# Optimization experiments

Hardware: AMD Instinct MI355X
Metric: run time of the kernel (lower is better)

## Reference

```python
import jax, jax.numpy as jnp
import numpy as np

N_HEAD = 16
N_FEAT = 1024
D_K = N_FEAT // N_HEAD
B, S = 2, 2048


def setup_inputs() -> dict:
    key = jax.random.key(0)
    ks = jax.random.split(key, 13)
    s = 1.0 / np.sqrt(N_FEAT)
    return {
        "query": jax.random.normal(ks[0], (B, S, N_FEAT), jnp.float32),
        "key": jax.random.normal(ks[1], (B, S, N_FEAT), jnp.float32),
        "value": jax.random.normal(ks[2], (B, S, N_FEAT), jnp.float32),
        "mask": jax.random.randint(ks[3], (B, 1, S), 0, 2).astype(bool),
        "w_q": jax.random.uniform(ks[4], (N_FEAT, N_FEAT), jnp.float32, -s, s),
        "b_q": jax.random.uniform(ks[5], (N_FEAT,), jnp.float32, -s, s),
        "w_k": jax.random.uniform(ks[6], (N_FEAT, N_FEAT), jnp.float32, -s, s),
        "b_k": jax.random.uniform(ks[7], (N_FEAT,), jnp.float32, -s, s),
        "w_v": jax.random.uniform(ks[8], (N_FEAT, N_FEAT), jnp.float32, -s, s),
        "b_v": jax.random.uniform(ks[9], (N_FEAT,), jnp.float32, -s, s),
        "w_o": jax.random.uniform(ks[10], (N_FEAT, N_FEAT), jnp.float32, -s, s),
        "b_o": jax.random.uniform(ks[11], (N_FEAT,), jnp.float32, -s, s),
    }


def reference(query, key, value, mask, w_q, b_q, w_k, b_k, w_v, b_v, w_o, b_o):
    b = query.shape[0]
    # projections -> [b, h, s, d_k]
    def proj(x, w, bias):
        y = x @ w.T + bias
        return y.reshape(b, -1, N_HEAD, D_K).transpose(0, 2, 1, 3)

    q = proj(query, w_q, b_q)
    k = proj(key, w_k, b_k)
    v = proj(value, w_v, b_v)

    scores = jnp.einsum("bhqd,bhkd->bhqk", q, k) / jnp.sqrt(jnp.asarray(D_K, q.dtype))
    m = mask[:, None]  # [b,1,1,s] broadcast over heads and query positions
    scores = jnp.where(m, jnp.asarray(-10000.0, scores.dtype), scores)
    attn = jax.nn.softmax(scores, axis=-1)
    attn = jnp.where(m, jnp.asarray(0.0, attn.dtype), attn)
    x = jnp.einsum("bhqk,bhkd->bhqd", attn, v)
    x = x.transpose(0, 2, 1, 3).reshape(b, -1, N_HEAD * D_K)
    return x @ w_o.T + b_o
```

## Files before the change

kernel.cpp:

```cpp
#include <hip/hip_runtime.h>
#include <hip/hip_bf16.h>


typedef float f32x4 __attribute__((ext_vector_type(4)));
typedef short bf16x8 __attribute__((ext_vector_type(8)));

typedef const __attribute__((address_space(1))) void* gas_ptr;
typedef __attribute__((address_space(3))) void* las_ptr;

#if __has_builtin(__builtin_amdgcn_exp2f)
#define EXP2(x) __builtin_amdgcn_exp2f(x)
#else
#define EXP2(x) exp2f(x)
#endif
#define LOG2E 1.4426950408889634f

static __device__ __forceinline__ short to_bf16s(float f) {
    __hip_bfloat16 h = __float2bfloat16(f);
    return __builtin_bit_cast(short, h);
}
static __device__ __forceinline__ unsigned cvtpk(float lo, float hi) {
    unsigned r;
    asm("v_cvt_pk_bf16_f32 %0, %1, %2" : "=v"(r) : "v"(lo), "v"(hi));
    return r;
}

__global__ void cvt3_kernel(const float* __restrict__ s0, const float* __restrict__ s1,
                            const float* __restrict__ s2, short* __restrict__ d0,
                            short* __restrict__ d1, short* __restrict__ d2) {
    const int g = blockIdx.x;
    const int sel = g >> 12;
    const int i = (g & 4095) * 256 + threadIdx.x;
    const float* s = sel == 0 ? s0 : (sel == 1 ? s1 : s2);
    short* d = sel == 0 ? d0 : (sel == 1 ? d1 : d2);
    float4 v = reinterpret_cast<const float4*>(s)[i];
    short4 o;
    o.x = to_bf16s(v.x); o.y = to_bf16s(v.y); o.z = to_bf16s(v.z); o.w = to_bf16s(v.w);
    reinterpret_cast<short4*>(d)[i] = o;
}
__global__ void cvt4_kernel(const float* __restrict__ s0, const float* __restrict__ s1,
                            const float* __restrict__ s2, const float* __restrict__ s3,
                            short* __restrict__ d0, short* __restrict__ d1,
                            short* __restrict__ d2, short* __restrict__ d3) {
    const int g = blockIdx.x;
    const int sel = g >> 10;
    const int i = (g & 1023) * 256 + threadIdx.x;
    const float* s = sel == 0 ? s0 : (sel == 1 ? s1 : (sel == 2 ? s2 : s3));
    short* d = sel == 0 ? d0 : (sel == 1 ? d1 : (sel == 2 ? d2 : d3));
    float4 v = reinterpret_cast<const float4*>(s)[i];
    short4 o;
    o.x = to_bf16s(v.x); o.y = to_bf16s(v.y); o.z = to_bf16s(v.z); o.w = to_bf16s(v.w);
    reinterpret_cast<short4*>(d)[i] = o;
}

__global__ void maskf_kernel(const int* __restrict__ mask, float* __restrict__ mf) {
    const int i = blockIdx.x * 256 + threadIdx.x;
    const int p = i & 31;
    const int phi = 8 * ((p >> 2) & 3) + 4 * (p >> 4) + (p & 3);
    mf[i] = mask[(i & ~31) | phi] ? (-10000.0f * LOG2E) : 0.0f;
}

static __device__ __forceinline__ void stage_tile(
    short* sa, short* sb, const short* A, const short* W,
    int m0, int n0, int k0, int tid)
{
#pragma unroll
    for (int rnd = 0; rnd < 2; ++rnd) {
        const int t = rnd * 256 + tid;
        const int c2 = t & 7;
        const int row = 2 * (t >> 3) + (c2 & 1);
        const int col = (c2 >> 1) * 8;
        __builtin_amdgcn_global_load_lds((gas_ptr)(A + (long)(m0 + row) * 1024 + k0 + col),
                                         (las_ptr)(sa + t * 8), 16, 0, 0);
        __builtin_amdgcn_global_load_lds((gas_ptr)(W + (long)(n0 + row) * 1024 + k0 + col),
                                         (las_ptr)(sb + t * 8), 16, 0, 0);
    }
}

static __device__ __forceinline__ void gemm_compute(
    const short* sa, const short* sb, int wr, int wc, int aoff, f32x4 (&acc)[4][4])
{
    bf16x8 af[4], bfr[4];
#pragma unroll
    for (int i = 0; i < 4; ++i)
        af[i] = *reinterpret_cast<const bf16x8*>(sa + (wr + i * 16) * 32 + aoff);
#pragma unroll
    for (int j = 0; j < 4; ++j)
        bfr[j] = *reinterpret_cast<const bf16x8*>(sb + (wc + j * 16) * 32 + aoff);
#pragma unroll
    for (int i = 0; i < 4; ++i)
#pragma unroll
        for (int j = 0; j < 4; ++j)
            acc[i][j] = __builtin_amdgcn_mfma_f32_16x16x32_bf16(af[i], bfr[j], acc[i][j], 0, 0, 0);
}

__global__ __launch_bounds__(256, 3) void proj_gemm(
    const short* __restrict__ A0, const short* __restrict__ A1, const short* __restrict__ A2,
    const short* __restrict__ W0, const short* __restrict__ W1, const short* __restrict__ W2,
    const float* __restrict__ bi0, const float* __restrict__ bi1, const float* __restrict__ bi2,
    short* __restrict__ o0, short* __restrict__ o1, short* __restrict__ o2)
{
    __shared__ __align__(16) short sa[2][4096];
    __shared__ __align__(16) short sb[2][4096];
    const int z = blockIdx.z;
    const short* A = z == 0 ? A0 : (z == 1 ? A1 : A2);
    const short* W = z == 0 ? W0 : (z == 1 ? W1 : W2);
    const float* bias = z == 0 ? bi0 : (z == 1 ? bi1 : bi2);
    short* outp = z == 0 ? o0 : (z == 1 ? o1 : o2);

    const int tid = threadIdx.x;
    const int w = tid >> 6, l = tid & 63;
    const int lr = l & 15, lh = l >> 4;
    const int m0 = blockIdx.x * 128, n0 = blockIdx.y * 128;
    const int wr = (w >> 1) * 64, wc = (w & 1) * 64;
    const int aoff = (lr >> 1) * 64 + (lr & 1) * 8 + lh * 16;

    f32x4 acc[4][4] = {};

    stage_tile(sa[0], sb[0], A, W, m0, n0, 0, tid);
    __syncthreads();
    for (int k0 = 0; k0 < 1024; k0 += 64) {
        stage_tile(sa[1], sb[1], A, W, m0, n0, k0 + 32, tid);
        gemm_compute(sa[0], sb[0], wr, wc, aoff, acc);
        __syncthreads();
        if (k0 + 64 < 1024)
            stage_tile(sa[0], sb[0], A, W, m0, n0, k0 + 64, tid);
        gemm_compute(sa[1], sb[1], wr, wc, aoff, acc);
        __syncthreads();
    }

    const float scl = (z == 0) ? 0.125f * LOG2E : 1.0f;
#pragma unroll
    for (int i = 0; i < 4; ++i) {
#pragma unroll
        for (int j = 0; j < 4; ++j) {
#pragma unroll
            for (int r = 0; r < 4; ++r) {
                const int row = m0 + wr + i * 16 + lh * 4 + r;
                const int col = n0 + wc + j * 16 + lr;
                const float v = (acc[i][j][r] + bias[col]) * scl;
                const int b = row >> 11, s = row & 2047;
                const int h = col >> 6, d = col & 63;
                if (z != 2)
                    outp[(((long)(b * 16 + h)) * 2048 + s) * 64 + d] = to_bf16s(v);
                else
                    outp[(((long)(b * 16 + h)) * 64 + d) * 2048 + s] = to_bf16s(v);
            }
        }
    }
}

__global__ __launch_bounds__(256, 2) void out_gemm(
    const short* __restrict__ A, const short* __restrict__ W,
    const float* __restrict__ bias, float* __restrict__ outp)
{
    __shared__ __align__(16) short sa[2][4096];
    __shared__ __align__(16) short sb[2][2048];
    const int tid = threadIdx.x;
    const int w = tid >> 6, l = tid & 63;
    const int lr = l & 15, lh = l >> 4;
    const int m0 = blockIdx.x * 128, n0 = blockIdx.y * 64;
    const int wr = (w >> 1) * 64, wc = (w & 1) * 32;
    const int aoff = (lr >> 1) * 64 + (lr & 1) * 8 + lh * 16;

    f32x4 acc[4][2] = {};

    const int c2 = tid & 7;
    const int brow = 2 * (tid >> 3) + (c2 & 1);
    const int bcol = (c2 >> 1) * 8;

    auto stage = [&](short* pa, short* pb, int k0) {
#pragma unroll
        for (int rnd = 0; rnd < 2; ++rnd) {
            const int t = rnd * 256 + tid;
            const int cc = t & 7;
            const int row = 2 * (t >> 3) + (cc & 1);
            const int col = (cc >> 1) * 8;
            __builtin_amdgcn_global_load_lds((gas_ptr)(A + (long)(m0 + row) * 1024 + k0 + col),
                                             (las_ptr)(pa + t * 8), 16, 0, 0);
        }
        __builtin_amdgcn_global_load_lds((gas_ptr)(W + (long)(n0 + brow) * 1024 + k0 + bcol),
                                         (las_ptr)(pb + tid * 8), 16, 0, 0);
    };
    auto compute = [&](const short* pa, const short* pb) {
        bf16x8 af[4], bfr[2];
#pragma unroll
        for (int i = 0; i < 4; ++i)
            af[i] = *reinterpret_cast<const bf16x8*>(pa + (wr + i * 16) * 32 + aoff);
#pragma unroll
        for (int j = 0; j < 2; ++j)
            bfr[j] = *reinterpret_cast<const bf16x8*>(pb + (wc + j * 16) * 32 + aoff);
#pragma unroll
        for (int i = 0; i < 4; ++i)
#pragma unroll
            for (int j = 0; j < 2; ++j)
                acc[i][j] = __builtin_amdgcn_mfma_f32_16x16x32_bf16(af[i], bfr[j], acc[i][j], 0, 0, 0);
    };

    stage(sa[0], sb[0], 0);
    __syncthreads();
    for (int k0 = 0; k0 < 1024; k0 += 64) {
        stage(sa[1], sb[1], k0 + 32);
        compute(sa[0], sb[0]);
        __syncthreads();
        if (k0 + 64 < 1024)
            stage(sa[0], sb[0], k0 + 64);
        compute(sa[1], sb[1]);
        __syncthreads();
    }

#pragma unroll
    for (int i = 0; i < 4; ++i)
#pragma unroll
        for (int j = 0; j < 2; ++j)
#pragma unroll
            for (int r = 0; r < 4; ++r) {
                const int row = m0 + wr + i * 16 + lh * 4 + r;
                const int col = n0 + wc + j * 16 + lr;
                outp[(long)row * 1024 + col] = acc[i][j][r] + bias[col];
            }
}


static __device__ __forceinline__ void stage_kv(
    short* ldsKb, short* ldsVb, const short* Kg, const short* Vg,
    int key0, int w, int srow, int prow, int schunk)
{
    __builtin_amdgcn_global_load_lds((gas_ptr)(Kg + (long)(key0 + prow) * 64 + schunk * 8),
                                     (las_ptr)(ldsKb + w * 512), 16, 0, 0);
    __builtin_amdgcn_global_load_lds((gas_ptr)(Kg + (long)(key0 + 32 + prow) * 64 + schunk * 8),
                                     (las_ptr)(ldsKb + 2048 + w * 512), 16, 0, 0);
    __builtin_amdgcn_global_load_lds((gas_ptr)(Vg + (long)srow * 2048 + key0 + schunk * 8),
                                     (las_ptr)(ldsVb + w * 512), 16, 0, 0);
    __builtin_amdgcn_global_load_lds((gas_ptr)(Vg + (long)(srow + 32) * 2048 + key0 + schunk * 8),
                                     (las_ptr)(ldsVb + 2048 + w * 512), 16, 0, 0);
}

static __device__ __forceinline__ void attn_step(
    const short* __restrict__ Kbuf, const short* __restrict__ Vbuf,
    const float* __restrict__ ldsM, int key0,
    const bf16x8 qf0, const bf16x8 qf1, int lr, int lh, int sw,
    float& mreg, float& lsum, f32x4 (&ao)[4])
{
    f32x4 mb[4];
#pragma unroll
    for (int s = 0; s < 4; ++s)
        mb[s] = *reinterpret_cast<const f32x4*>(ldsM + key0 + s * 16 + lh * 4);

    f32x4 sc[4];
#pragma unroll
    for (int s = 0; s < 4; ++s) {
        const short* kb = Kbuf + (s * 16 + lr) * 64;
        bf16x8 k0 = *reinterpret_cast<const bf16x8*>(kb + (((lh * 16) ^ sw) >> 1));
        bf16x8 k1 = *reinterpret_cast<const bf16x8*>(kb + (((64 + lh * 16) ^ sw) >> 1));
        sc[s] = __builtin_amdgcn_mfma_f32_16x16x32_bf16(k0, qf0, mb[s], 0, 0, 0);
        sc[s] = __builtin_amdgcn_mfma_f32_16x16x32_bf16(k1, qf1, sc[s], 0, 0, 0);
    }

    float m0 = fmaxf(fmaxf(fmaxf(sc[0][0], sc[0][1]), sc[0][2]), sc[0][3]);
    float m1 = fmaxf(fmaxf(fmaxf(sc[1][0], sc[1][1]), sc[1][2]), sc[1][3]);
    float m2 = fmaxf(fmaxf(fmaxf(sc[2][0], sc[2][1]), sc[2][2]), sc[2][3]);
    float m3 = fmaxf(fmaxf(fmaxf(sc[3][0], sc[3][1]), sc[3][2]), sc[3][3]);
    float t = fmaxf(fmaxf(m0, m1), fmaxf(m2, m3));
    t = fmaxf(t, __shfl_xor(t, 16));
    t = fmaxf(t, __shfl_xor(t, 32));
    if (__any(t > mreg + 8.0f)) {
        const float mn = fmaxf(mreg, t);
        const float sf = EXP2(mreg - mn);
        lsum *= sf;
#pragma unroll
        for (int d4 = 0; d4 < 4; ++d4) ao[d4] *= sf;
        mreg = mn;
    }
    float p[16], ps = 0.f;
#pragma unroll
    for (int s = 0; s < 4; ++s) {
#pragma unroll
        for (int r = 0; r < 4; ++r) {
            const float e = EXP2(sc[s][r] - mreg);
            p[s * 4 + r] = e;
            ps += e;
        }
    }
    ps += __shfl_xor(ps, 16);
    ps += __shfl_xor(ps, 32);
    lsum += ps;

    unsigned pw[8];
#pragma unroll
    for (int i = 0; i < 8; ++i) pw[i] = cvtpk(p[2 * i], p[2 * i + 1]);
    const bf16x8 pb0 = __builtin_bit_cast(bf16x8, *(ulonglong2*)&pw[0]);
    const bf16x8 pb1 = __builtin_bit_cast(bf16x8, *(ulonglong2*)&pw[4]);

#pragma unroll
    for (int c = 0; c < 2; ++c) {
        const bf16x8 pbc = c == 0 ? pb0 : pb1;
#pragma unroll
        for (int d4 = 0; d4 < 4; ++d4) {
            const short* vb = Vbuf + (d4 * 16 + lr) * 64;
            bf16x8 vf = *reinterpret_cast<const bf16x8*>(vb + (((c * 64 + lh * 16) ^ sw) >> 1));
            ao[d4] = __builtin_amdgcn_mfma_f32_16x16x32_bf16(vf, pbc, ao[d4], 0, 0, 0);
        }
    }
}

__global__ __launch_bounds__(256, 4) void attn_kernel(
    const short* __restrict__ Q, const short* __restrict__ Kmat,
    const short* __restrict__ Vt, const float* __restrict__ maskf,
    short* __restrict__ X)
{
    __shared__ __align__(16) short ldsK[2][4096];
    __shared__ __align__(16) short ldsV[2][4096];
    __shared__ __align__(16) float ldsM[2048];

    const int id = blockIdx.x;
    const int slot = id >> 3;
    const int bh = (id & 7) * 4 + (slot >> 5);
    const int q0 = (slot & 31) * 64;
    const int b = bh >> 4, h = bh & 15;
    const int w = threadIdx.x >> 6, l = threadIdx.x & 63;
    const int lr = l & 15, lh = l >> 4;
    const int sw = (lr & 7) << 4;

    const int srow = w * 8 + (l >> 3);
    const int schunk = (l & 7) ^ (srow & 7);
    const int prow = 8 * ((srow >> 2) & 3) + 4 * (srow >> 4) + (srow & 3);

    const short* Kg = Kmat + (long)bh * 2048 * 64;
    const short* Vg = Vt + (long)bh * 64 * 2048;

#pragma unroll
    for (int rnd = 0; rnd < 2; ++rnd) {
        const int t = rnd * 256 + threadIdx.x;
        __builtin_amdgcn_global_load_lds((gas_ptr)(maskf + (long)b * 2048 + t * 4),
                                         (las_ptr)(ldsM + t * 4), 16, 0, 0);
    }

    const short* Qp = Q + ((long)bh * 2048 + q0 + w * 16 + lr) * 64 + lh * 8;
    const bf16x8 qf0 = *reinterpret_cast<const bf16x8*>(Qp);
    const bf16x8 qf1 = *reinterpret_cast<const bf16x8*>(Qp + 32);

    float mreg = -1e30f, lsum = 0.f;
    f32x4 ao[4] = {};

    stage_kv(ldsK[0], ldsV[0], Kg, Vg, 0, w, srow, prow, schunk);
    __syncthreads();

    for (int tt = 0; tt < 16; ++tt) {
        const int key0 = tt * 128;
        stage_kv(ldsK[1], ldsV[1], Kg, Vg, key0 + 64, w, srow, prow, schunk);
        attn_step(ldsK[0], ldsV[0], ldsM, key0, qf0, qf1, lr, lh, sw, mreg, lsum, ao);
        __syncthreads();
        if (tt < 15)
            stage_kv(ldsK[0], ldsV[0], Kg, Vg, key0 + 128, w, srow, prow, schunk);
        attn_step(ldsK[1], ldsV[1], ldsM, key0 + 64, qf0, qf1, lr, lh, sw, mreg, lsum, ao);
        __syncthreads();
    }

    const float inv = 1.0f / fmaxf(lsum, 1e-30f);
    const int s = q0 + w * 16 + lr;
    short* Xp = X + ((long)b * 2048 + s) * 1024 + h * 64 + lh * 4;
#pragma unroll
    for (int d4 = 0; d4 < 4; ++d4) {
        uint2 o;
        o.x = cvtpk(ao[d4][0] * inv, ao[d4][1] * inv);
        o.y = cvtpk(ao[d4][2] * inv, ao[d4][3] * inv);
        *reinterpret_cast<uint2*>(Xp + d4 * 16) = o;
    }
}

extern "C" void kernel_launch(void* const* d_in, const int* in_sizes, int n_in,
                              void* d_out, int out_size, void* d_ws, size_t ws_size,
                              hipStream_t stream) {
    const float* query = (const float*)d_in[0];
    const float* key_  = (const float*)d_in[1];
    const float* value = (const float*)d_in[2];
    const int*   mask  = (const int*)d_in[3];
    const float* w_q = (const float*)d_in[4];
    const float* b_q = (const float*)d_in[5];
    const float* w_k = (const float*)d_in[6];
    const float* b_k = (const float*)d_in[7];
    const float* w_v = (const float*)d_in[8];
    const float* b_v = (const float*)d_in[9];
    const float* w_o = (const float*)d_in[10];
    const float* b_o = (const float*)d_in[11];

    const long SEQ = 4194304;
    const long WSZ = 1048576;
    short* ws = (short*)d_ws;
    short* cq = ws;
    short* ck = cq + SEQ;
    short* cv = ck + SEQ;
    short* wq = cv + SEQ;
    short* wk = wq + WSZ;
    short* wv = wk + WSZ;
    short* wo = wv + WSZ;
    short* Qb = wo + WSZ;
    short* Kb = Qb + SEQ;
    short* Vt = Kb + SEQ;
    short* Xb = cq;
    float* mkf = (float*)cv;

    cvt3_kernel<<<12288, 256, 0, stream>>>(query, key_, value, cq, ck, cv);
    cvt4_kernel<<<4096, 256, 0, stream>>>(w_q, w_k, w_v, w_o, wq, wk, wv, wo);

    dim3 blk(256);
    proj_gemm<<<dim3(32, 8, 3), blk, 0, stream>>>(cq, ck, cv, wq, wk, wv,
                                                  b_q, b_k, b_v, Qb, Kb, Vt);

    maskf_kernel<<<16, 256, 0, stream>>>(mask, mkf);

    attn_kernel<<<1024, blk, 0, stream>>>(Qb, Kb, Vt, mkf, Xb);

    out_gemm<<<dim3(32, 16), blk, 0, stream>>>(Xb, wo, b_o, (float*)d_out);
}
```

Measured before the change: 142.3 us.

## Transpose V projection output through LDS and prefetch mask into registers

The V projection epilogue previously wrote scattered 2-byte transposed stores. It now stages the tile transposed in shared memory and writes contiguous 4-byte rows along the sequence dimension for coalescing. The attention kernel drops its LDS mask buffer and loads mask values straight from global memory into registers, double-buffered alongside the K/V staging, which frees LDS and may raise occupancy. The softmax sums are also restructured into tree reductions to shorten dependency chains. The changes add an extra barrier and an enlarged shared array in proj_gemm, plus more registers in attn_kernel.

```diff
diff --git a/kernel.cpp b/kernel.cpp
--- a/kernel.cpp
+++ b/kernel.cpp
@@ -100,8 +100,12 @@
     const float* __restrict__ bi0, const float* __restrict__ bi1, const float* __restrict__ bi2,
     short* __restrict__ o0, short* __restrict__ o1, short* __restrict__ o2)
 {
-    __shared__ __align__(16) short sa[2][4096];
-    __shared__ __align__(16) short sb[2][4096];
+    __shared__ __align__(16) short smem[17408];
+    short* sA0 = smem;
+    short* sA1 = smem + 4096;
+    short* sB0 = smem + 8192;
+    short* sB1 = smem + 12288;
+
     const int z = blockIdx.z;
     const short* A = z == 0 ? A0 : (z == 1 ? A1 : A2);
     const short* W = z == 0 ? W0 : (z == 1 ? W1 : W2);
@@ -117,35 +121,59 @@
 
     f32x4 acc[4][4] = {};
 
-    stage_tile(sa[0], sb[0], A, W, m0, n0, 0, tid);
+    stage_tile(sA0, sB0, A, W, m0, n0, 0, tid);
     __syncthreads();
     for (int k0 = 0; k0 < 1024; k0 += 64) {
-        stage_tile(sa[1], sb[1], A, W, m0, n0, k0 + 32, tid);
-        gemm_compute(sa[0], sb[0], wr, wc, aoff, acc);
+        stage_tile(sA1, sB1, A, W, m0, n0, k0 + 32, tid);
+        gemm_compute(sA0, sB0, wr, wc, aoff, acc);
         __syncthreads();
         if (k0 + 64 < 1024)
-            stage_tile(sa[0], sb[0], A, W, m0, n0, k0 + 64, tid);
-        gemm_compute(sa[1], sb[1], wr, wc, aoff, acc);
-        __syncthreads();
-    }
-
-    const float scl = (z == 0) ? 0.125f * LOG2E : 1.0f;
-#pragma unroll
-    for (int i = 0; i < 4; ++i) {
-#pragma unroll
-        for (int j = 0; j < 4; ++j) {
-#pragma unroll
-            for (int r = 0; r < 4; ++r) {
-                const int row = m0 + wr + i * 16 + lh * 4 + r;
-                const int col = n0 + wc + j * 16 + lr;
-                const float v = (acc[i][j][r] + bias[col]) * scl;
-                const int b = row >> 11, s = row & 2047;
-                const int h = col >> 6, d = col & 63;
-                if (z != 2)
+            stage_tile(sA0, sB0, A, W, m0, n0, k0 + 64, tid);
+        gemm_compute(sA1, sB1, wr, wc, aoff, acc);
+        __syncthreads();
+    }
+
+    if (z != 2) {
+        const float scl = (z == 0) ? 0.125f * LOG2E : 1.0f;
+#pragma unroll
+        for (int i = 0; i < 4; ++i) {
+#pragma unroll
+            for (int j = 0; j < 4; ++j) {
+#pragma unroll
+                for (int r = 0; r < 4; ++r) {
+                    const int row = m0 + wr + i * 16 + lh * 4 + r;
+                    const int col = n0 + wc + j * 16 + lr;
+                    const float v = (acc[i][j][r] + bias[col]) * scl;
+                    const int b = row >> 11, s = row & 2047;
+                    const int h = col >> 6, d = col & 63;
                     outp[(((long)(b * 16 + h)) * 2048 + s) * 64 + d] = to_bf16s(v);
-                else
-                    outp[(((long)(b * 16 + h)) * 64 + d) * 2048 + s] = to_bf16s(v);
+                }
             }
+        }
+    } else {
+#pragma unroll
+        for (int i = 0; i < 4; ++i) {
+#pragma unroll
+            for (int j = 0; j < 4; ++j) {
+                const int dl = wc + j * 16 + lr;
+                const int sl = wr + i * 16 + lh * 4;
+                const float bv = bias[n0 + dl];
+                const unsigned w0 = cvtpk(acc[i][j][0] + bv, acc[i][j][1] + bv);
+                const unsigned w1 = cvtpk(acc[i][j][2] + bv, acc[i][j][3] + bv);
+                uint2 pr; pr.x = w0; pr.y = w1;
+                *reinterpret_cast<uint2*>(smem + dl * 136 + sl) = pr;
+            }
+        }
+        __syncthreads();
+        const int bb = m0 >> 11;
+        const int s0 = m0 & 2047;
+#pragma unroll 4
+        for (int rr = 0; rr < 32; ++rr) {
+            const int dl = w * 32 + rr;
+            const int col = n0 + dl;
+            const int hh = col >> 6, dd = col & 63;
+            const unsigned val = *reinterpret_cast<const unsigned*>(smem + dl * 136 + 2 * l);
+            *reinterpret_cast<unsigned*>(outp + ((long)(bb * 16 + hh) * 64 + dd) * 2048 + s0 + 2 * l) = val;
         }
     }
 }
@@ -238,15 +266,10 @@
 
 static __device__ __forceinline__ void attn_step(
     const short* __restrict__ Kbuf, const short* __restrict__ Vbuf,
-    const float* __restrict__ ldsM, int key0,
+    const f32x4 (&mb)[4],
     const bf16x8 qf0, const bf16x8 qf1, int lr, int lh, int sw,
     float& mreg, float& lsum, f32x4 (&ao)[4])
 {
-    f32x4 mb[4];
-#pragma unroll
-    for (int s = 0; s < 4; ++s)
-        mb[s] = *reinterpret_cast<const f32x4*>(ldsM + key0 + s * 16 + lh * 4);
-
     f32x4 sc[4];
 #pragma unroll
     for (int s = 0; s < 4; ++s) {
@@ -257,10 +280,10 @@
         sc[s] = __builtin_amdgcn_mfma_f32_16x16x32_bf16(k1, qf1, sc[s], 0, 0, 0);
     }
 
-    float m0 = fmaxf(fmaxf(fmaxf(sc[0][0], sc[0][1]), sc[0][2]), sc[0][3]);
-    float m1 = fmaxf(fmaxf(fmaxf(sc[1][0], sc[1][1]), sc[1][2]), sc[1][3]);
-    float m2 = fmaxf(fmaxf(fmaxf(sc[2][0], sc[2][1]), sc[2][2]), sc[2][3]);
-    float m3 = fmaxf(fmaxf(fmaxf(sc[3][0], sc[3][1]), sc[3][2]), sc[3][3]);
+    float m0 = fmaxf(fmaxf(sc[0][0], sc[0][1]), fmaxf(sc[0][2], sc[0][3]));
+    float m1 = fmaxf(fmaxf(sc[1][0], sc[1][1]), fmaxf(sc[1][2], sc[1][3]));
+    float m2 = fmaxf(fmaxf(sc[2][0], sc[2][1]), fmaxf(sc[2][2], sc[2][3]));
+    float m3 = fmaxf(fmaxf(sc[3][0], sc[3][1]), fmaxf(sc[3][2], sc[3][3]));
     float t = fmaxf(fmaxf(m0, m1), fmaxf(m2, m3));
     t = fmaxf(t, __shfl_xor(t, 16));
     t = fmaxf(t, __shfl_xor(t, 32));
@@ -272,23 +295,24 @@
         for (int d4 = 0; d4 < 4; ++d4) ao[d4] *= sf;
         mreg = mn;
     }
-    float p[16], ps = 0.f;
-#pragma unroll
-    for (int s = 0; s < 4; ++s) {
-#pragma unroll
-        for (int r = 0; r < 4; ++r) {
-            const float e = EXP2(sc[s][r] - mreg);
-            p[s * 4 + r] = e;
-            ps += e;
-        }
-    }
+    float e[16];
+#pragma unroll
+    for (int s = 0; s < 4; ++s)
+#pragma unroll
+        for (int r = 0; r < 4; ++r)
+            e[s * 4 + r] = EXP2(sc[s][r] - mreg);
+    const float e0 = (e[0] + e[1]) + (e[2] + e[3]);
+    const float e1 = (e[4] + e[5]) + (e[6] + e[7]);
+    const float e2 = (e[8] + e[9]) + (e[10] + e[11]);
+    const float e3 = (e[12] + e[13]) + (e[14] + e[15]);
+    float ps = (e0 + e1) + (e2 + e3);
     ps += __shfl_xor(ps, 16);
     ps += __shfl_xor(ps, 32);
     lsum += ps;
 
     unsigned pw[8];
 #pragma unroll
-    for (int i = 0; i < 8; ++i) pw[i] = cvtpk(p[2 * i], p[2 * i + 1]);
+    for (int i = 0; i < 8; ++i) pw[i] = cvtpk(e[2 * i], e[2 * i + 1]);
     const bf16x8 pb0 = __builtin_bit_cast(bf16x8, *(ulonglong2*)&pw[0]);
     const bf16x8 pb1 = __builtin_bit_cast(bf16x8, *(ulonglong2*)&pw[4]);
 
@@ -311,7 +335,6 @@
 {
     __shared__ __align__(16) short ldsK[2][4096];
     __shared__ __align__(16) short ldsV[2][4096];
-    __shared__ __align__(16) float ldsM[2048];
 
     const int id = blockIdx.x;
     const int slot = id >> 3;
@@ -328,13 +351,7 @@
 
     const short* Kg = Kmat + (long)bh * 2048 * 64;
     const short* Vg = Vt + (long)bh * 64 * 2048;
-
-#pragma unroll
-    for (int rnd = 0; rnd < 2; ++rnd) {
-        const int t = rnd * 256 + threadIdx.x;
-        __builtin_amdgcn_global_load_lds((gas_ptr)(maskf + (long)b * 2048 + t * 4),
-                                         (las_ptr)(ldsM + t * 4), 16, 0, 0);
-    }
+    const float* mfp = maskf + b * 2048 + lh * 4;
 
     const short* Qp = Q + ((long)bh * 2048 + q0 + w * 16 + lr) * 64 + lh * 8;
     const bf16x8 qf0 = *reinterpret_cast<const bf16x8*>(Qp);
@@ -343,17 +360,29 @@
     float mreg = -1e30f, lsum = 0.f;
     f32x4 ao[4] = {};
 
+    f32x4 mbA[4], mbB[4];
+#pragma unroll
+    for (int s = 0; s < 4; ++s)
+        mbA[s] = *reinterpret_cast<const f32x4*>(mfp + s * 16);
+
     stage_kv(ldsK[0], ldsV[0], Kg, Vg, 0, w, srow, prow, schunk);
     __syncthreads();
 
     for (int tt = 0; tt < 16; ++tt) {
         const int key0 = tt * 128;
+#pragma unroll
+        for (int s = 0; s < 4; ++s)
+            mbB[s] = *reinterpret_cast<const f32x4*>(mfp + key0 + 64 + s * 16);
         stage_kv(ldsK[1], ldsV[1], Kg, Vg, key0 + 64, w, srow, prow, schunk);
-        attn_step(ldsK[0], ldsV[0], ldsM, key0, qf0, qf1, lr, lh, sw, mreg, lsum, ao);
-        __syncthreads();
-        if (tt < 15)
+        attn_step(ldsK[0], ldsV[0], mbA, qf0, qf1, lr, lh, sw, mreg, lsum, ao);
+        __syncthreads();
+        if (tt < 15) {
+#pragma unroll
+            for (int s = 0; s < 4; ++s)
+                mbA[s] = *reinterpret_cast<const f32x4*>(mfp + key0 + 128 + s * 16);
             stage_kv(ldsK[0], ldsV[0], Kg, Vg, key0 + 128, w, srow, prow, schunk);
-        attn_step(ldsK[1], ldsV[1], ldsM, key0 + 64, qf0, qf1, lr, lh, sw, mreg, lsum, ao);
+        }
+        attn_step(ldsK[1], ldsV[1], mbB, qf0, qf1, lr, lh, sw, mreg, lsum, ao);
         __syncthreads();
     }
 
```

After: 139.1 us, median of 3. 1.02x faster.
